# Kernel optimization log

Measured on AMD Instinct MI355X. Metric: run time of the kernel, lower is better.

The kernel has to match this reference:

```python
import jax, jax.numpy as jnp
import numpy as np


def setup_inputs() -> dict:
    key = jax.random.key(0)
    ks = jax.random.split(key, 5)
    N, T, D, H = 256, 64, 1024, 1024
    x = jax.random.normal(ks[0], (N, T, D), dtype=jnp.float32)
    A = jax.random.normal(ks[1], (N, H, 4, 4), dtype=jnp.float32)
    Wx = jax.random.normal(ks[2], (D, 4 * H), dtype=jnp.float32) / np.sqrt(D)
    Wh = jax.random.normal(ks[3], (H, 4 * H), dtype=jnp.float32) / np.sqrt(H)
    Wattn = jax.random.normal(ks[4], (H, 4 * H), dtype=jnp.float32) / np.sqrt(H)
    b = jnp.zeros((4 * H,), dtype=jnp.float32)
    return {"x": x, "A": A, "Wx": Wx, "Wh": Wh, "Wattn": Wattn, "b": b}


def reference(x, A, Wx, Wh, Wattn, b):
    # x: (N,T,D); A: (N,H,4,4); Wx: (D,4H); Wh,Wattn: (H,4H); b: (4H,)
    N, T, D = x.shape
    H = A.shape[1]
    A_flat = A.reshape(N, H, 16)                 # 16 = 4*4 spatial keys
    h0 = A_flat.mean(axis=2)                     # (N,H); c0 = h0
    scale = 1.0 / jnp.sqrt(jnp.asarray(H, dtype=x.dtype))

    def step(carry, xt):
        prev_h, prev_c = carry
        # scaled dot-product attention over 16 spatial positions
        scores = jnp.einsum('nh,nhk->nk', prev_h, A_flat) * scale   # (N,16)
        w = jax.nn.softmax(scores, axis=1)                           # (N,16)
        attn = jnp.einsum('nhk,nk->nh', A_flat, w)                   # (N,H)
        # LSTM gates with attention term
        a = xt @ Wx + prev_h @ Wh + attn @ Wattn + b                 # (N,4H)
        ai, af, ao, ag = jnp.split(a, 4, axis=1)
        i = jax.nn.sigmoid(ai)
        f = jax.nn.sigmoid(af)
        o = jax.nn.sigmoid(ao)
        g = jnp.tanh(ag)
        next_c = f * prev_c + i * g
        next_h = o * jnp.tanh(next_c)
        return (next_h, next_c), next_h

    xs = jnp.swapaxes(x, 0, 1)                   # (T,N,D)
    _, hs = jax.lax.scan(step, (h0, h0), xs)     # hs: (T,N,H)
    return jnp.swapaxes(hs, 0, 1)                # (N,T,H)
```

## Files before the change

kernel.cpp:

```cpp
#include <hip/hip_runtime.h>
#include <math.h>

#define NB 256
#define TT 64
#define DD 1024
#define HH 1024
#define FOURH 4096
#define KTOT 3072
#define KT16 192
#define P1 (NB * FOURH)
#define NZ 8

#define AF_LVL 786432ull
#define BF_LVL 12582912ull
#define SPLIT_SCALE 2048.0f
#define INV_SPLIT (1.0f / 2048.0f)

typedef _Float16 f16x8 __attribute__((ext_vector_type(8)));
typedef float f32x4 __attribute__((ext_vector_type(4)));
typedef float f32x16 __attribute__((ext_vector_type(16)));

__device__ __forceinline__ unsigned short f2h(float f) {
    _Float16 h = (_Float16)f;
    unsigned short u;
    __builtin_memcpy(&u, &h, 2);
    return u;
}
__device__ __forceinline__ float h2f(unsigned short u) {
    _Float16 h;
    __builtin_memcpy(&h, &u, 2);
    return (float)h;
}
__device__ __forceinline__ void split2(float f, unsigned short& hi, unsigned short& lo) {
    hi = f2h(f);
    lo = f2h((f - h2f(hi)) * SPLIT_SCALE);
}

__device__ __forceinline__ size_t aoff(int lvl, int mt, int kt, int lane) {
    return ((size_t)((lvl * 8 + mt) * KT16 + kt) * 64 + lane) * 8;
}
__device__ __forceinline__ size_t boff(int lvl, int ct, int kt, int lane) {
    return ((size_t)((lvl * 128 + ct) * KT16 + kt) * 64 + lane) * 8;
}

__device__ __forceinline__ void write_frag8(unsigned short* __restrict__ Af, int n, int k8, const float* v) {
    int mt = n >> 5, kt = k8 >> 4;
    int lane = (n & 31) + 32 * ((k8 >> 3) & 1);
    unsigned short s[8][2];
#pragma unroll
    for (int i = 0; i < 8; ++i) split2(v[i], s[i][0], s[i][1]);
#pragma unroll
    for (int lvl = 0; lvl < 2; ++lvl) {
        uint4 p;
        p.x = (unsigned)s[0][lvl] | ((unsigned)s[1][lvl] << 16);
        p.y = (unsigned)s[2][lvl] | ((unsigned)s[3][lvl] << 16);
        p.z = (unsigned)s[4][lvl] | ((unsigned)s[5][lvl] << 16);
        p.w = (unsigned)s[6][lvl] | ((unsigned)s[7][lvl] << 16);
        *reinterpret_cast<uint4*>(Af + aoff(lvl, mt, kt, lane)) = p;
    }
}

__global__ __launch_bounds__(256) void wsplit_kernel(const float* __restrict__ Wx,
                                                     const float* __restrict__ Wh,
                                                     const float* __restrict__ Wattn,
                                                     unsigned short* __restrict__ Bf) {
    __shared__ float tile[32][33];
    int k0 = blockIdx.x * 32, j0 = blockIdx.y * 32;
    int t = threadIdx.x;
    int rl = t >> 3, c4 = (t & 7) * 4;
    int seg = k0 >> 10;
    const float* W = (seg == 0) ? Wx : (seg == 1) ? Wh : Wattn;
    const float4 v = *reinterpret_cast<const float4*>(W + (size_t)((k0 & 1023) + rl) * FOURH + j0 + c4);
    tile[rl][c4 + 0] = v.x; tile[rl][c4 + 1] = v.y; tile[rl][c4 + 2] = v.z; tile[rl][c4 + 3] = v.w;
    __syncthreads();
    int jl = t >> 3, k4 = (t & 7) * 4;
    unsigned short s[4][2];
#pragma unroll
    for (int i = 0; i < 4; ++i) split2(tile[k4 + i][jl], s[i][0], s[i][1]);
    int j = j0 + jl;
    int kg = k0 + k4;
    int ct = j >> 5, kt = kg >> 4;
    int lane = (j & 31) + 32 * ((kg >> 3) & 1);
    int sub = kg & 7;
#pragma unroll
    for (int lvl = 0; lvl < 2; ++lvl) {
        uint2 p;
        p.x = (unsigned)s[0][lvl] | ((unsigned)s[1][lvl] << 16);
        p.y = (unsigned)s[2][lvl] | ((unsigned)s[3][lvl] << 16);
        *reinterpret_cast<uint2*>(Bf + boff(lvl, ct, kt, lane) + sub) = p;
    }
}

__device__ __forceinline__ void attn_phase(const float* __restrict__ A, int n, int tid,
                                           const float* hsh, float* ash, float* red2) {
    int lane = tid & 63, wave = tid >> 6;
    const float* An = A + (size_t)n * HH * 16;
    float areg[2][16];
    float part[16];
#pragma unroll
    for (int k = 0; k < 16; ++k) part[k] = 0.f;
#pragma unroll
    for (int i = 0; i < 2; ++i) {
        int hh = tid + i * 512;
        float hv = hsh[hh];
        const float* ap = An + (size_t)hh * 16;
#pragma unroll
        for (int k = 0; k < 16; ++k) {
            float av = ap[k];
            areg[i][k] = av;
            part[k] += hv * av;
        }
    }
#pragma unroll
    for (int k = 0; k < 16; ++k) {
        float v = part[k];
#pragma unroll
        for (int off = 32; off > 0; off >>= 1) v += __shfl_down(v, off);
        if (lane == 0) red2[wave * 16 + k] = v;
    }
    __syncthreads();
    float w[16];
    float mx = -1e30f;
#pragma unroll
    for (int k = 0; k < 16; ++k) {
        float s = 0.f;
#pragma unroll
        for (int q = 0; q < 8; ++q) s += red2[q * 16 + k];
        s *= 0.03125f;
        w[k] = s;
        mx = fmaxf(mx, s);
    }
    float sum = 0.f;
#pragma unroll
    for (int k = 0; k < 16; ++k) {
        w[k] = expf(w[k] - mx);
        sum += w[k];
    }
    float inv = 1.0f / sum;
#pragma unroll
    for (int k = 0; k < 16; ++k) w[k] *= inv;
#pragma unroll
    for (int i = 0; i < 2; ++i) {
        float s = 0.f;
#pragma unroll
        for (int k = 0; k < 16; ++k) s += areg[i][k] * w[k];
        ash[tid + i * 512] = s;
    }
}

__device__ __forceinline__ void write_state_frags(unsigned short* __restrict__ Af,
                                                  const float* __restrict__ x,
                                                  const float* hsh, const float* ash,
                                                  int n, int tnext, int tid) {
    int seg = tid >> 7;
    int k8 = (tid & 127) * 8;
    float v[8];
    if (seg == 0) {
#pragma unroll
        for (int i = 0; i < 8; ++i) v[i] = hsh[k8 + i];
        write_frag8(Af, n, 1024 + k8, v);
    } else if (seg == 1) {
#pragma unroll
        for (int i = 0; i < 8; ++i) v[i] = ash[k8 + i];
        write_frag8(Af, n, 2048 + k8, v);
    } else if (seg == 2 && tnext < TT) {
        const float4* xp = reinterpret_cast<const float4*>(x + ((size_t)n * TT + tnext) * DD + k8);
        float4 x0 = xp[0], x1 = xp[1];
        v[0] = x0.x; v[1] = x0.y; v[2] = x0.z; v[3] = x0.w;
        v[4] = x1.x; v[5] = x1.y; v[6] = x1.z; v[7] = x1.w;
        write_frag8(Af, n, k8, v);
    }
}

__global__ __launch_bounds__(512) void initk(const float* __restrict__ A,
                                             const float* __restrict__ x,
                                             float* __restrict__ c,
                                             unsigned short* __restrict__ Af) {
    int n = blockIdx.x, tid = threadIdx.x;
    __shared__ float hsh[HH], ash[HH];
    __shared__ float red2[128];
#pragma unroll
    for (int i = 0; i < 2; ++i) {
        int hh = tid + i * 512;
        const float* ap = A + ((size_t)n * HH + hh) * 16;
        float s = 0.f;
#pragma unroll
        for (int k = 0; k < 16; ++k) s += ap[k];
        s *= (1.0f / 16.0f);
        c[(size_t)n * HH + hh] = s;
        hsh[hh] = s;
    }
    __syncthreads();
    attn_phase(A, n, tid, hsh, ash, red2);
    __syncthreads();
    write_state_frags(Af, x, hsh, ash, n, 0, tid);
}

#define KTPB 24
#define NCHUNK 12
#define BUFS 20480

#define STAGE(bidx, cc)                                                                        \
    {                                                                                          \
        _Pragma("unroll") for (int j = 0; j < 5; ++j) {                                        \
            __builtin_amdgcn_global_load_lds(                                                  \
                (const __attribute__((address_space(1))) unsigned int*)(sb[j] + (size_t)(cc) * 1024), \
                (__attribute__((address_space(3))) unsigned int*)&Bsm[(bidx)][ldsoff[j]],      \
                16, 0, 0);                                                                     \
        }                                                                                      \
    }

__global__ __launch_bounds__(512) void gemm_mfma(const unsigned short* __restrict__ Af,
                                                 const unsigned short* __restrict__ Bf,
                                                 float* __restrict__ apart) {
    __shared__ __align__(16) unsigned short Bsm[2][BUFS];
    int tid = threadIdx.x;
    int l = tid & 63, w = tid >> 6;
    int wm = w & 3, wn = w >> 2;
    int bid = blockIdx.x;
    int id = ((bid & 7) << 6) + (bid >> 3);
    int colb = id & 63, z = id >> 6;
    int kt0 = z * KTPB;

    const unsigned short* sb[5];
    int ldsoff[5];
#pragma unroll
    for (int j = 0; j < 5; ++j) {
        int f = w + 8 * j;
        if (f < 32) {
            int ktc = f >> 4, lvl = (f >> 3) & 1, mt = f & 7;
            sb[j] = Af + aoff(lvl, mt, kt0 + ktc, l);
        } else {
            int g = f - 32;
            int ktc = g >> 2, lvl = (g >> 1) & 1, ct = g & 1;
            sb[j] = Bf + boff(lvl, colb * 2 + ct, kt0 + ktc, l);
        }
        ldsoff[j] = f * 512;
    }

    f32x16 accH[2] = {};
    f32x16 accM[2] = {};

    STAGE(0, 0)
    STAGE(1, 1)

    for (int cc = 0; cc < NCHUNK; ++cc) {
        if (cc + 1 < NCHUNK) { asm volatile("s_waitcnt vmcnt(5)" ::: "memory"); }
        else                 { asm volatile("s_waitcnt vmcnt(0)" ::: "memory"); }
        __builtin_amdgcn_sched_barrier(0);
        __builtin_amdgcn_s_barrier();
        __builtin_amdgcn_sched_barrier(0);

        const unsigned short* base = &Bsm[cc & 1][0];
        __builtin_amdgcn_s_setprio(1);
#pragma unroll
        for (int ktc = 0; ktc < 2; ++ktc) {
            const unsigned short* bp = base + (size_t)(32 + ktc * 4 + wn) * 512 + l * 8;
            f16x8 b0 = *reinterpret_cast<const f16x8*>(bp);
            f16x8 b1 = *reinterpret_cast<const f16x8*>(bp + 1024);
            const unsigned short* ap0 = base + (size_t)(ktc * 16 + wm * 2) * 512 + l * 8;
            f16x8 a0m0 = *reinterpret_cast<const f16x8*>(ap0);
            f16x8 a0m1 = *reinterpret_cast<const f16x8*>(ap0 + 512);
            f16x8 a1m0 = *reinterpret_cast<const f16x8*>(ap0 + 8 * 512);
            f16x8 a1m1 = *reinterpret_cast<const f16x8*>(ap0 + 9 * 512);
            accH[0] = __builtin_amdgcn_mfma_f32_32x32x16_f16(a0m0, b0, accH[0], 0, 0, 0);
            accM[0] = __builtin_amdgcn_mfma_f32_32x32x16_f16(a0m0, b1, accM[0], 0, 0, 0);
            accM[0] = __builtin_amdgcn_mfma_f32_32x32x16_f16(a1m0, b0, accM[0], 0, 0, 0);
            accH[1] = __builtin_amdgcn_mfma_f32_32x32x16_f16(a0m1, b0, accH[1], 0, 0, 0);
            accM[1] = __builtin_amdgcn_mfma_f32_32x32x16_f16(a0m1, b1, accM[1], 0, 0, 0);
            accM[1] = __builtin_amdgcn_mfma_f32_32x32x16_f16(a1m1, b0, accM[1], 0, 0, 0);
        }
        __builtin_amdgcn_s_setprio(0);

        __builtin_amdgcn_sched_barrier(0);
        __builtin_amdgcn_s_barrier();
        if (cc + 2 < NCHUNK) STAGE(cc & 1, cc + 2)
    }

    float* plane = apart + (size_t)z * P1;
    int col = colb * 64 + wn * 32 + (l & 31);
#pragma unroll
    for (int mi = 0; mi < 2; ++mi) {
        int rbase = (wm * 2 + mi) * 32 + (l >> 5) * 4;
#pragma unroll
        for (int r = 0; r < 16; ++r) {
            int row = rbase + (r & 3) + 8 * (r >> 2);
            plane[(size_t)row * FOURH + col] = accH[mi][r] + accM[mi][r] * INV_SPLIT;
        }
    }
}

__global__ __launch_bounds__(512) void pointwise(const float* __restrict__ apart,
                                                 const float* __restrict__ bias,
                                                 const float* __restrict__ A,
                                                 const float* __restrict__ x,
                                                 float* __restrict__ c,
                                                 float* __restrict__ out,
                                                 unsigned short* __restrict__ Af, int t) {
    int n = blockIdx.x, tid = threadIdx.x;
    __shared__ float hsh[HH], ash[HH];
    __shared__ float red2[128];
    const float* ap = apart + (size_t)n * FOURH;
    int hh2 = tid * 2;
    float2 g2[4];
#pragma unroll
    for (int g = 0; g < 4; ++g) {
        int j = g * 1024 + hh2;
        float2 s = *reinterpret_cast<const float2*>(bias + j);
#pragma unroll
        for (int zz = 0; zz < NZ; ++zz) {
            float2 p = *reinterpret_cast<const float2*>(ap + (size_t)zz * P1 + j);
            s.x += p.x; s.y += p.y;
        }
        g2[g] = s;
    }
    float2 cold = *reinterpret_cast<const float2*>(c + (size_t)n * HH + hh2);
    float2 hn2;
    {
        float ig = 1.f / (1.f + expf(-g2[0].x));
        float fg = 1.f / (1.f + expf(-g2[1].x));
        float og = 1.f / (1.f + expf(-g2[2].x));
        float gg = tanhf(g2[3].x);
        float cn = fg * cold.x + ig * gg;
        hn2.x = og * tanhf(cn);
        cold.x = cn;
    }
    {
        float ig = 1.f / (1.f + expf(-g2[0].y));
        float fg = 1.f / (1.f + expf(-g2[1].y));
        float og = 1.f / (1.f + expf(-g2[2].y));
        float gg = tanhf(g2[3].y);
        float cn = fg * cold.y + ig * gg;
        hn2.y = og * tanhf(cn);
        cold.y = cn;
    }
    *reinterpret_cast<float2*>(c + (size_t)n * HH + hh2) = cold;
    *reinterpret_cast<float2*>(out + ((size_t)n * TT + t) * HH + hh2) = hn2;
    *reinterpret_cast<float2*>(&hsh[hh2]) = hn2;
    __syncthreads();
    attn_phase(A, n, tid, hsh, ash, red2);
    __syncthreads();
    write_state_frags(Af, x, hsh, ash, n, t + 1, tid);
}

extern "C" void kernel_launch(void* const* d_in, const int* in_sizes, int n_in,
                              void* d_out, int out_size, void* d_ws, size_t ws_size,
                              hipStream_t stream) {
    const float* x     = (const float*)d_in[0];
    const float* A     = (const float*)d_in[1];
    const float* Wx    = (const float*)d_in[2];
    const float* Wh    = (const float*)d_in[3];
    const float* Wattn = (const float*)d_in[4];
    const float* b     = (const float*)d_in[5];
    float* out = (float*)d_out;

    unsigned short* Bf = (unsigned short*)d_ws;
    unsigned short* Af = Bf + 2 * BF_LVL;
    float* apart = (float*)(Af + 2 * AF_LVL);
    float* c = apart + (size_t)NZ * P1;

    wsplit_kernel<<<dim3(KTOT / 32, FOURH / 32), 256, 0, stream>>>(Wx, Wh, Wattn, Bf);
    initk<<<NB, 512, 0, stream>>>(A, x, c, Af);

    for (int t = 0; t < TT; ++t) {
        gemm_mfma<<<512, 512, 0, stream>>>(Af, Bf, apart);
        pointwise<<<NB, 512, 0, stream>>>(apart, b, A, x, c, out, Af, t);
    }
}
```

Before: 2.797 ms.

## Fuse LSTM gate pointwise into GEMM via last-block split-K reduction

Weight columns are permuted so each 64-column GEMM tile holds all four gates for 16 hidden units. This lets the last of the split-K blocks for a tile, detected with an atomic counter, reduce the partials and apply the LSTM cell update in place. Split-K drops from 8 to 4 with a grid of 256 blocks and a triple-buffered LDS pipeline that issues the prefetch before compute. The attention and x-fragment work moves to a smaller kernel, and Af is double-buffered so the GEMM can write the next h while the current step is still read. The intent is to cut partial-sum traffic and pointwise work, at the cost of less K parallelism, fewer blocks, and added atomic and threadfence overhead.

```diff
diff --git a/kernel.cpp b/kernel.cpp
--- a/kernel.cpp
+++ b/kernel.cpp
@@ -8,8 +8,7 @@
 #define FOURH 4096
 #define KTOT 3072
 #define KT16 192
-#define P1 (NB * FOURH)
-#define NZ 8
+#define NZ 4
 
 #define AF_LVL 786432ull
 #define BF_LVL 12582912ull
@@ -17,7 +16,6 @@
 #define INV_SPLIT (1.0f / 2048.0f)
 
 typedef _Float16 f16x8 __attribute__((ext_vector_type(8)));
-typedef float f32x4 __attribute__((ext_vector_type(4)));
 typedef float f32x16 __attribute__((ext_vector_type(16)));
 
 __device__ __forceinline__ unsigned short f2h(float f) {
@@ -78,9 +76,10 @@
 #pragma unroll
     for (int i = 0; i < 4; ++i) split2(tile[k4 + i][jl], s[i][0], s[i][1]);
     int j = j0 + jl;
+    int jn = ((j & 1023) << 2) | (j >> 10);
     int kg = k0 + k4;
-    int ct = j >> 5, kt = kg >> 4;
-    int lane = (j & 31) + 32 * ((kg >> 3) & 1);
+    int ct = jn >> 5, kt = kg >> 4;
+    int lane = (jn & 31) + 32 * ((kg >> 3) & 1);
     int sub = kg & 7;
 #pragma unroll
     for (int lvl = 0; lvl < 2; ++lvl) {
@@ -175,10 +174,12 @@
 __global__ __launch_bounds__(512) void initk(const float* __restrict__ A,
                                              const float* __restrict__ x,
                                              float* __restrict__ c,
-                                             unsigned short* __restrict__ Af) {
+                                             unsigned short* __restrict__ Af0,
+                                             int* __restrict__ cnt) {
     int n = blockIdx.x, tid = threadIdx.x;
     __shared__ float hsh[HH], ash[HH];
     __shared__ float red2[128];
+    if (n == 0 && tid < 64) cnt[tid] = 0;
 #pragma unroll
     for (int i = 0; i < 2; ++i) {
         int hh = tid + i * 512;
@@ -193,11 +194,11 @@
     __syncthreads();
     attn_phase(A, n, tid, hsh, ash, red2);
     __syncthreads();
-    write_state_frags(Af, x, hsh, ash, n, 0, tid);
-}
-
-#define KTPB 24
-#define NCHUNK 12
+    write_state_frags(Af0, x, hsh, ash, n, 0, tid);
+}
+
+#define KTPB 48
+#define NCHUNK 24
 #define BUFS 20480
 
 #define STAGE(bidx, cc)                                                                        \
@@ -210,15 +211,22 @@
         }                                                                                      \
     }
 
-__global__ __launch_bounds__(512) void gemm_mfma(const unsigned short* __restrict__ Af,
-                                                 const unsigned short* __restrict__ Bf,
-                                                 float* __restrict__ apart) {
-    __shared__ __align__(16) unsigned short Bsm[2][BUFS];
+__global__ __launch_bounds__(512) void gemm_fused(const unsigned short* __restrict__ Afr,
+                                                  const unsigned short* __restrict__ Bf,
+                                                  float* __restrict__ apart2,
+                                                  const float* __restrict__ bias,
+                                                  float* __restrict__ c,
+                                                  float* __restrict__ h,
+                                                  float* __restrict__ out,
+                                                  unsigned short* __restrict__ Afw,
+                                                  int* __restrict__ cnt, int t) {
+    __shared__ __align__(16) unsigned short Bsm[3][BUFS];
+    __shared__ int isLast;
     int tid = threadIdx.x;
     int l = tid & 63, w = tid >> 6;
     int wm = w & 3, wn = w >> 2;
     int bid = blockIdx.x;
-    int id = ((bid & 7) << 6) + (bid >> 3);
+    int id = ((bid & 7) << 5) + (bid >> 3);
     int colb = id & 63, z = id >> 6;
     int kt0 = z * KTPB;
 
@@ -229,7 +237,7 @@
         int f = w + 8 * j;
         if (f < 32) {
             int ktc = f >> 4, lvl = (f >> 3) & 1, mt = f & 7;
-            sb[j] = Af + aoff(lvl, mt, kt0 + ktc, l);
+            sb[j] = Afr + aoff(lvl, mt, kt0 + ktc, l);
         } else {
             int g = f - 32;
             int ktc = g >> 2, lvl = (g >> 1) & 1, ct = g & 1;
@@ -244,14 +252,19 @@
     STAGE(0, 0)
     STAGE(1, 1)
 
+    int cb = 0;
     for (int cc = 0; cc < NCHUNK; ++cc) {
         if (cc + 1 < NCHUNK) { asm volatile("s_waitcnt vmcnt(5)" ::: "memory"); }
         else                 { asm volatile("s_waitcnt vmcnt(0)" ::: "memory"); }
         __builtin_amdgcn_sched_barrier(0);
         __builtin_amdgcn_s_barrier();
         __builtin_amdgcn_sched_barrier(0);
-
-        const unsigned short* base = &Bsm[cc & 1][0];
+        if (cc + 2 < NCHUNK) {
+            int tb = cb + 2; if (tb >= 3) tb -= 3;
+            STAGE(tb, cc + 2)
+        }
+
+        const unsigned short* base = &Bsm[cb][0];
         __builtin_amdgcn_s_setprio(1);
 #pragma unroll
         for (int ktc = 0; ktc < 2; ++ktc) {
@@ -271,76 +284,96 @@
             accM[1] = __builtin_amdgcn_mfma_f32_32x32x16_f16(a1m1, b0, accM[1], 0, 0, 0);
         }
         __builtin_amdgcn_s_setprio(0);
-
-        __builtin_amdgcn_sched_barrier(0);
-        __builtin_amdgcn_s_barrier();
-        if (cc + 2 < NCHUNK) STAGE(cc & 1, cc + 2)
-    }
-
-    float* plane = apart + (size_t)z * P1;
-    int col = colb * 64 + wn * 32 + (l & 31);
-#pragma unroll
-    for (int mi = 0; mi < 2; ++mi) {
-        int rbase = (wm * 2 + mi) * 32 + (l >> 5) * 4;
-#pragma unroll
-        for (int r = 0; r < 16; ++r) {
-            int row = rbase + (r & 3) + 8 * (r >> 2);
-            plane[(size_t)row * FOURH + col] = accH[mi][r] + accM[mi][r] * INV_SPLIT;
-        }
-    }
-}
-
-__global__ __launch_bounds__(512) void pointwise(const float* __restrict__ apart,
-                                                 const float* __restrict__ bias,
-                                                 const float* __restrict__ A,
+        cb = (cb + 1 == 3) ? 0 : cb + 1;
+    }
+
+    {
+        float* slice = apart2 + ((size_t)(z * 64 + colb) * 256) * 64;
+        int col = wn * 32 + (l & 31);
+#pragma unroll
+        for (int mi = 0; mi < 2; ++mi) {
+            int rbase = (wm * 2 + mi) * 32 + (l >> 5) * 4;
+#pragma unroll
+            for (int r = 0; r < 16; ++r) {
+                int row = rbase + (r & 3) + 8 * (r >> 2);
+                slice[(size_t)row * 64 + col] = accH[mi][r] + accM[mi][r] * INV_SPLIT;
+            }
+        }
+    }
+
+    __threadfence();
+    __syncthreads();
+    if (tid == 0) {
+        int old = atomicAdd(&cnt[colb], 1);
+        isLast = (old == 3) ? 1 : 0;
+        if (old == 3) cnt[colb] = 0;
+    }
+    __syncthreads();
+    if (!isLast) return;
+    __threadfence();
+
+    int n = tid & 255, half = tid >> 8;
+    float qx[8], qy[8], qz[8], qw[8];
+#pragma unroll
+    for (int i = 0; i < 8; ++i) { qx[i] = 0.f; qy[i] = 0.f; qz[i] = 0.f; qw[i] = 0.f; }
+#pragma unroll
+    for (int zz = 0; zz < NZ; ++zz) {
+        const float4* sl = reinterpret_cast<const float4*>(
+            apart2 + ((size_t)(zz * 64 + colb) * 256 + n) * 64 + half * 32);
+#pragma unroll
+        for (int i = 0; i < 8; ++i) {
+            float4 q = sl[i];
+            qx[i] += q.x; qy[i] += q.y; qz[i] += q.z; qw[i] += q.w;
+        }
+    }
+    float hn8[8];
+#pragma unroll
+    for (int i = 0; i < 8; ++i) {
+        int hg = colb * 16 + half * 8 + i;
+        float ai = qx[i] + bias[hg];
+        float af = qy[i] + bias[1024 + hg];
+        float ao = qz[i] + bias[2048 + hg];
+        float ag = qw[i] + bias[3072 + hg];
+        float ig = 1.f / (1.f + expf(-ai));
+        float fg = 1.f / (1.f + expf(-af));
+        float og = 1.f / (1.f + expf(-ao));
+        float gg = tanhf(ag);
+        float cn = fg * c[(size_t)n * HH + hg] + ig * gg;
+        float hn = og * tanhf(cn);
+        c[(size_t)n * HH + hg] = cn;
+        out[((size_t)n * TT + t) * HH + hg] = hn;
+        h[(size_t)n * HH + hg] = hn;
+        hn8[i] = hn;
+    }
+    write_frag8(Afw, n, 1024 + colb * 16 + half * 8, hn8);
+}
+
+__global__ __launch_bounds__(512) void attn_mini(const float* __restrict__ A,
+                                                 const float* __restrict__ h,
                                                  const float* __restrict__ x,
-                                                 float* __restrict__ c,
-                                                 float* __restrict__ out,
-                                                 unsigned short* __restrict__ Af, int t) {
+                                                 unsigned short* __restrict__ Afw, int t) {
     int n = blockIdx.x, tid = threadIdx.x;
     __shared__ float hsh[HH], ash[HH];
     __shared__ float red2[128];
-    const float* ap = apart + (size_t)n * FOURH;
-    int hh2 = tid * 2;
-    float2 g2[4];
-#pragma unroll
-    for (int g = 0; g < 4; ++g) {
-        int j = g * 1024 + hh2;
-        float2 s = *reinterpret_cast<const float2*>(bias + j);
-#pragma unroll
-        for (int zz = 0; zz < NZ; ++zz) {
-            float2 p = *reinterpret_cast<const float2*>(ap + (size_t)zz * P1 + j);
-            s.x += p.x; s.y += p.y;
-        }
-        g2[g] = s;
-    }
-    float2 cold = *reinterpret_cast<const float2*>(c + (size_t)n * HH + hh2);
-    float2 hn2;
-    {
-        float ig = 1.f / (1.f + expf(-g2[0].x));
-        float fg = 1.f / (1.f + expf(-g2[1].x));
-        float og = 1.f / (1.f + expf(-g2[2].x));
-        float gg = tanhf(g2[3].x);
-        float cn = fg * cold.x + ig * gg;
-        hn2.x = og * tanhf(cn);
-        cold.x = cn;
-    }
-    {
-        float ig = 1.f / (1.f + expf(-g2[0].y));
-        float fg = 1.f / (1.f + expf(-g2[1].y));
-        float og = 1.f / (1.f + expf(-g2[2].y));
-        float gg = tanhf(g2[3].y);
-        float cn = fg * cold.y + ig * gg;
-        hn2.y = og * tanhf(cn);
-        cold.y = cn;
-    }
-    *reinterpret_cast<float2*>(c + (size_t)n * HH + hh2) = cold;
-    *reinterpret_cast<float2*>(out + ((size_t)n * TT + t) * HH + hh2) = hn2;
-    *reinterpret_cast<float2*>(&hsh[hh2]) = hn2;
+    hsh[tid] = h[(size_t)n * HH + tid];
+    hsh[tid + 512] = h[(size_t)n * HH + tid + 512];
     __syncthreads();
     attn_phase(A, n, tid, hsh, ash, red2);
     __syncthreads();
-    write_state_frags(Af, x, hsh, ash, n, t + 1, tid);
+    int seg = tid >> 7;
+    int k8 = (tid & 127) * 8;
+    float v[8];
+    if (seg == 0) {
+#pragma unroll
+        for (int i = 0; i < 8; ++i) v[i] = ash[k8 + i];
+        write_frag8(Afw, n, 2048 + k8, v);
+    } else if (seg == 1 && t + 1 < TT) {
+        const float4* xp = reinterpret_cast<const float4*>(x + ((size_t)n * TT + t + 1) * DD + k8);
+        float4 x0 = xp[0], x1 = xp[1];
+        v[0] = x0.x; v[1] = x0.y; v[2] = x0.z; v[3] = x0.w;
+        v[4] = x1.x; v[5] = x1.y; v[6] = x1.z; v[7] = x1.w;
+        write_frag8(Afw, n, k8, v);
+    }
 }
 
 extern "C" void kernel_launch(void* const* d_in, const int* in_sizes, int n_in,
@@ -354,16 +387,21 @@
     const float* b     = (const float*)d_in[5];
     float* out = (float*)d_out;
 
-    unsigned short* Bf = (unsigned short*)d_ws;
-    unsigned short* Af = Bf + 2 * BF_LVL;
-    float* apart = (float*)(Af + 2 * AF_LVL);
-    float* c = apart + (size_t)NZ * P1;
+    unsigned short* Bf  = (unsigned short*)d_ws;
+    unsigned short* Af0 = Bf + 2 * BF_LVL;
+    unsigned short* Af1 = Af0 + 2 * AF_LVL;
+    float* apart2 = (float*)(Af1 + 2 * AF_LVL);
+    float* c = apart2 + (size_t)NZ * 64 * 256 * 64;
+    float* h = c + (size_t)NB * HH;
+    int* cnt = (int*)(h + (size_t)NB * HH);
 
     wsplit_kernel<<<dim3(KTOT / 32, FOURH / 32), 256, 0, stream>>>(Wx, Wh, Wattn, Bf);
-    initk<<<NB, 512, 0, stream>>>(A, x, c, Af);
+    initk<<<NB, 512, 0, stream>>>(A, x, c, Af0, cnt);
 
     for (int t = 0; t < TT; ++t) {
-        gemm_mfma<<<512, 512, 0, stream>>>(Af, Bf, apart);
-        pointwise<<<NB, 512, 0, stream>>>(apart, b, A, x, c, out, Af, t);
-    }
-}
+        unsigned short* Afr = (t & 1) ? Af1 : Af0;
+        unsigned short* Afw = (t & 1) ? Af0 : Af1;
+        gemm_fused<<<256, 512, 0, stream>>>(Afr, Bf, apart2, b, c, h, out, Afw, cnt, t);
+        attn_mini<<<NB, 512, 0, stream>>>(A, h, x, Afw, t);
+    }
+}
```

Result: slower. 9.274 ms (+231.6%).

## Widen GEMM block tile to 128 columns and halve grid size

Applied to the files above, without the earlier changes.

Each GEMM workgroup now computes a 256x128 output tile instead of 256x64, so every A fragment loaded into LDS is reused across twice as many columns. The grid drops from 512 to 256 blocks, and staging grows to six global-to-LDS loads per chunk, with more LDS and twice the accumulators per wave. The aim is to cut redundant A-matrix traffic per step. The cost is fewer blocks on the GPU, which may underfill the 256 CUs, and higher register pressure.

```diff
diff --git a/kernel.cpp b/kernel.cpp
--- a/kernel.cpp
+++ b/kernel.cpp
@@ -17,7 +17,6 @@
 #define INV_SPLIT (1.0f / 2048.0f)
 
 typedef _Float16 f16x8 __attribute__((ext_vector_type(8)));
-typedef float f32x4 __attribute__((ext_vector_type(4)));
 typedef float f32x16 __attribute__((ext_vector_type(16)));
 
 __device__ __forceinline__ unsigned short f2h(float f) {
@@ -198,11 +197,11 @@
 
 #define KTPB 24
 #define NCHUNK 12
-#define BUFS 20480
+#define BUFS 24576
 
 #define STAGE(bidx, cc)                                                                        \
     {                                                                                          \
-        _Pragma("unroll") for (int j = 0; j < 5; ++j) {                                        \
+        _Pragma("unroll") for (int j = 0; j < 6; ++j) {                                        \
             __builtin_amdgcn_global_load_lds(                                                  \
                 (const __attribute__((address_space(1))) unsigned int*)(sb[j] + (size_t)(cc) * 1024), \
                 (__attribute__((address_space(3))) unsigned int*)&Bsm[(bidx)][ldsoff[j]],      \
@@ -218,34 +217,34 @@
     int l = tid & 63, w = tid >> 6;
     int wm = w & 3, wn = w >> 2;
     int bid = blockIdx.x;
-    int id = ((bid & 7) << 6) + (bid >> 3);
-    int colb = id & 63, z = id >> 6;
+    int id = ((bid & 7) << 5) + (bid >> 3);
+    int colb = id & 31, z = id >> 5;
     int kt0 = z * KTPB;
 
-    const unsigned short* sb[5];
-    int ldsoff[5];
-#pragma unroll
-    for (int j = 0; j < 5; ++j) {
+    const unsigned short* sb[6];
+    int ldsoff[6];
+#pragma unroll
+    for (int j = 0; j < 6; ++j) {
         int f = w + 8 * j;
         if (f < 32) {
             int ktc = f >> 4, lvl = (f >> 3) & 1, mt = f & 7;
             sb[j] = Af + aoff(lvl, mt, kt0 + ktc, l);
         } else {
             int g = f - 32;
-            int ktc = g >> 2, lvl = (g >> 1) & 1, ct = g & 1;
-            sb[j] = Bf + boff(lvl, colb * 2 + ct, kt0 + ktc, l);
+            int ktc = g >> 3, lvl = (g >> 2) & 1, ct = g & 3;
+            sb[j] = Bf + boff(lvl, colb * 4 + ct, kt0 + ktc, l);
         }
         ldsoff[j] = f * 512;
     }
 
-    f32x16 accH[2] = {};
-    f32x16 accM[2] = {};
+    f32x16 accH[2][2] = {};
+    f32x16 accM[2][2] = {};
 
     STAGE(0, 0)
     STAGE(1, 1)
 
     for (int cc = 0; cc < NCHUNK; ++cc) {
-        if (cc + 1 < NCHUNK) { asm volatile("s_waitcnt vmcnt(5)" ::: "memory"); }
+        if (cc + 1 < NCHUNK) { asm volatile("s_waitcnt vmcnt(6)" ::: "memory"); }
         else                 { asm volatile("s_waitcnt vmcnt(0)" ::: "memory"); }
         __builtin_amdgcn_sched_barrier(0);
         __builtin_amdgcn_s_barrier();
@@ -255,20 +254,31 @@
         __builtin_amdgcn_s_setprio(1);
 #pragma unroll
         for (int ktc = 0; ktc < 2; ++ktc) {
-            const unsigned short* bp = base + (size_t)(32 + ktc * 4 + wn) * 512 + l * 8;
-            f16x8 b0 = *reinterpret_cast<const f16x8*>(bp);
-            f16x8 b1 = *reinterpret_cast<const f16x8*>(bp + 1024);
             const unsigned short* ap0 = base + (size_t)(ktc * 16 + wm * 2) * 512 + l * 8;
-            f16x8 a0m0 = *reinterpret_cast<const f16x8*>(ap0);
-            f16x8 a0m1 = *reinterpret_cast<const f16x8*>(ap0 + 512);
-            f16x8 a1m0 = *reinterpret_cast<const f16x8*>(ap0 + 8 * 512);
-            f16x8 a1m1 = *reinterpret_cast<const f16x8*>(ap0 + 9 * 512);
-            accH[0] = __builtin_amdgcn_mfma_f32_32x32x16_f16(a0m0, b0, accH[0], 0, 0, 0);
-            accM[0] = __builtin_amdgcn_mfma_f32_32x32x16_f16(a0m0, b1, accM[0], 0, 0, 0);
-            accM[0] = __builtin_amdgcn_mfma_f32_32x32x16_f16(a1m0, b0, accM[0], 0, 0, 0);
-            accH[1] = __builtin_amdgcn_mfma_f32_32x32x16_f16(a0m1, b0, accH[1], 0, 0, 0);
-            accM[1] = __builtin_amdgcn_mfma_f32_32x32x16_f16(a0m1, b1, accM[1], 0, 0, 0);
-            accM[1] = __builtin_amdgcn_mfma_f32_32x32x16_f16(a1m1, b0, accM[1], 0, 0, 0);
+            f16x8 a0[2], a1[2];
+            a0[0] = *reinterpret_cast<const f16x8*>(ap0);
+            a0[1] = *reinterpret_cast<const f16x8*>(ap0 + 512);
+            a1[0] = *reinterpret_cast<const f16x8*>(ap0 + 8 * 512);
+            a1[1] = *reinterpret_cast<const f16x8*>(ap0 + 9 * 512);
+            const unsigned short* bp0 = base + (size_t)(32 + ktc * 8 + wn * 2) * 512 + l * 8;
+            f16x8 b0[2], b1[2];
+            b0[0] = *reinterpret_cast<const f16x8*>(bp0);
+            b0[1] = *reinterpret_cast<const f16x8*>(bp0 + 512);
+            b1[0] = *reinterpret_cast<const f16x8*>(bp0 + 4 * 512);
+            b1[1] = *reinterpret_cast<const f16x8*>(bp0 + 5 * 512);
+#pragma unroll
+            for (int mi = 0; mi < 2; ++mi) {
+                f16x8 aH = (mi == 0) ? a0[0] : a0[1];
+                f16x8 aL = (mi == 0) ? a1[0] : a1[1];
+#pragma unroll
+                for (int ni = 0; ni < 2; ++ni) {
+                    f16x8 bH = (ni == 0) ? b0[0] : b0[1];
+                    f16x8 bL = (ni == 0) ? b1[0] : b1[1];
+                    accH[mi][ni] = __builtin_amdgcn_mfma_f32_32x32x16_f16(aH, bH, accH[mi][ni], 0, 0, 0);
+                    accM[mi][ni] = __builtin_amdgcn_mfma_f32_32x32x16_f16(aH, bL, accM[mi][ni], 0, 0, 0);
+                    accM[mi][ni] = __builtin_amdgcn_mfma_f32_32x32x16_f16(aL, bH, accM[mi][ni], 0, 0, 0);
+                }
+            }
         }
         __builtin_amdgcn_s_setprio(0);
 
@@ -278,14 +288,17 @@
     }
 
     float* plane = apart + (size_t)z * P1;
-    int col = colb * 64 + wn * 32 + (l & 31);
 #pragma unroll
     for (int mi = 0; mi < 2; ++mi) {
         int rbase = (wm * 2 + mi) * 32 + (l >> 5) * 4;
 #pragma unroll
-        for (int r = 0; r < 16; ++r) {
-            int row = rbase + (r & 3) + 8 * (r >> 2);
-            plane[(size_t)row * FOURH + col] = accH[mi][r] + accM[mi][r] * INV_SPLIT;
+        for (int ni = 0; ni < 2; ++ni) {
+            int col = colb * 128 + (wn * 2 + ni) * 32 + (l & 31);
+#pragma unroll
+            for (int r = 0; r < 16; ++r) {
+                int row = rbase + (r & 3) + 8 * (r >> 2);
+                plane[(size_t)row * FOURH + col] = accH[mi][ni][r] + accM[mi][ni][r] * INV_SPLIT;
+            }
         }
     }
 }
@@ -363,7 +376,7 @@
     initk<<<NB, 512, 0, stream>>>(A, x, c, Af);
 
     for (int t = 0; t < TT; ++t) {
-        gemm_mfma<<<512, 512, 0, stream>>>(Af, Bf, apart);
+        gemm_mfma<<<256, 512, 0, stream>>>(Af, Bf, apart);
         pointwise<<<NB, 512, 0, stream>>>(apart, b, A, x, c, out, Af, t);
     }
 }
```

After: 2.694 ms. 3.7% less time.
